# Performance work log

Measured on AMD Instinct MI355X. Metric: run time of the kernel, lower is better.

## Reference

```python
import jax, jax.numpy as jnp
import numpy as np

N = 100000   # nodes (single node type 'A')
C = 256      # hidden_channels
OUT = 128    # out_channels
E_RAND = 300000  # random edges; total E = N + E_RAND = 400000
LN_EPS = 1e-5


def _linear_params(key, in_c, out_c):
    kw, kb = jax.random.split(key)
    bound = 1.0 / np.sqrt(in_c)
    W = jax.random.uniform(kw, (out_c, in_c), minval=-bound, maxval=bound, dtype=jnp.float32)
    b = jax.random.uniform(kb, (out_c,), minval=-bound, maxval=bound, dtype=jnp.float32)
    return W, b


def _edges(key):
    # guarantee every node appears in both rows -> unique()/remap in the torch
    # code is the identity, so the subgraph equals the full graph
    k0, k1 = jax.random.split(key)
    base = jnp.arange(N, dtype=jnp.int64)
    row0 = jnp.concatenate([base, jax.random.randint(k0, (E_RAND,), 0, N, dtype=jnp.int64)])
    row1 = jnp.concatenate([base, jax.random.randint(k1, (E_RAND,), 0, N, dtype=jnp.int64)])
    return jnp.stack([row0, row1])


def setup_inputs() -> dict:
    key = jax.random.key(0)
    ks = jax.random.split(key, 12)
    x = jax.random.normal(ks[0], (N, C), dtype=jnp.float32)
    edge_index_r0 = _edges(ks[1])
    edge_index_r1 = _edges(ks[2])
    wl0, bl0 = _linear_params(ks[3], C, C)
    w00, b00 = _linear_params(ks[4], C, C)
    w10, b10 = _linear_params(ks[5], C, C)
    wl1, bl1 = _linear_params(ks[6], C, C)
    w01, b01 = _linear_params(ks[7], C, C)
    w11, b11 = _linear_params(ks[8], C, C)
    Wout, bout = _linear_params(ks[9], C, OUT)
    return dict(
        x=x, edge_index_r0=edge_index_r0, edge_index_r1=edge_index_r1,
        wl0=wl0, bl0=bl0, w00=w00, b00=b00, w10=w10, b10=b10,
        gate0=jnp.float32(0.5), lns0=jnp.ones((C,), jnp.float32), lnb0=jnp.zeros((C,), jnp.float32),
        wl1=wl1, bl1=bl1, w01=w01, b01=b01, w11=w11, b11=b11,
        gate1=jnp.float32(0.5), lns1=jnp.ones((C,), jnp.float32), lnb1=jnp.zeros((C,), jnp.float32),
        Wout=Wout, bout=bout,
    )


def _metapath_layer(x0, h, ei, wl, bl, w0, b0, w1, b1, gate, lns, lnb):
    n = h.shape[0]
    src, dst = ei[0], ei[1]
    # PyG flow='target_to_source', aggr='add': message x_j = h[edge_index[1]],
    # scatter-added at edge_index[0]
    agg = jax.ops.segment_sum(h[dst], src, num_segments=n)
    # original code normalizes by bincount of edge_index[1] (kept faithfully)
    deg = jax.ops.segment_sum(jnp.ones_like(dst, dtype=h.dtype), dst, num_segments=n)
    agg = agg / jnp.clip(deg, 1.0)[:, None]
    g = jax.nn.sigmoid(gate)
    out = (agg @ wl.T + bl) + (1.0 - g) * (h @ w0.T + b0) + g * (x0 @ w1.T + b1)
    out = jax.nn.relu(out)
    mu = out.mean(-1, keepdims=True)
    var = out.var(-1, keepdims=True)
    out = (out - mu) / jnp.sqrt(var + LN_EPS) * lns + lnb
    return out  # dropout is identity in eval mode


def reference(x, edge_index_r0, edge_index_r1,
              wl0, bl0, w00, b00, w10, b10, gate0, lns0, lnb0,
              wl1, bl1, w01, b01, w11, b11, gate1, lns1, lnb1,
              Wout, bout):
    x0 = jax.lax.stop_gradient(x)  # x0_dict is detached in the torch code
    h = x
    # metapath is processed in reverse: conv index 1 first, then conv index 0
    h = _metapath_layer(x0, h, edge_index_r1, wl1, bl1, w01, b01, w11, b11, gate1, lns1, lnb1)
    h = _metapath_layer(x0, h, edge_index_r0, wl0, bl0, w00, b00, w10, b10, gate0, lns0, lnb0)
    return h @ Wout.T + bout
```

## Files before the change

### kernel.cpp

```cpp
#include <hip/hip_runtime.h>

typedef unsigned short u16;
typedef unsigned int   u32;

typedef __attribute__((ext_vector_type(8))) __bf16 bf16x8;
typedef __attribute__((ext_vector_type(8))) unsigned short u16x8;
typedef __attribute__((ext_vector_type(4))) float  f32x4;

#define C      256
#define KCAT   768
#define OUTC   128
#define LN_EPS 1e-5f

__device__ __forceinline__ float bf2f(u16 u) {
    u32 i = ((u32)u) << 16; float f; __builtin_memcpy(&f, &i, 4); return f;
}
__device__ __forceinline__ u16 f2bf(float f) {
    u32 i; __builtin_memcpy(&i, &f, 4);
    u32 r = (i + 0x7FFFu + ((i >> 16) & 1u)) >> 16;
    return (u16)r;
}
__device__ __forceinline__ void load_lds16(const void* g, void* l) {
    __builtin_amdgcn_global_load_lds((const __attribute__((address_space(1))) u32*)g,
                                     (__attribute__((address_space(3))) u32*)l, 16, 0, 0);
}

__global__ void prep_weights(const float* wlA, const float* w0A, const float* w1A,
                             const float* blA, const float* b0A, const float* b1A,
                             const float* gateA,
                             const float* wlB, const float* w0B, const float* w1B,
                             const float* blB, const float* b0B, const float* b1B,
                             const float* gateB,
                             const float* Wout,
                             u16* __restrict__ Wcat, float* __restrict__ bcat,
                             u16* __restrict__ Woutb)
{
    int idx = blockIdx.x * 256 + threadIdx.x;
    if (idx < 2 * C * KCAT) {
        int L   = idx / (C * KCAT);
        int rem = idx - L * (C * KCAT);
        int n   = rem / KCAT;
        int k   = rem - n * KCAT;
        const float* wl = L ? wlB : wlA;
        const float* w0 = L ? w0B : w0A;
        const float* w1 = L ? w1B : w1A;
        float g = 1.f / (1.f + expf(-((L ? gateB : gateA)[0])));
        float v;
        if (k < 256)      v = wl[n * 256 + k];
        else if (k < 512) v = (1.f - g) * w0[n * 256 + (k - 256)];
        else              v = g * w1[n * 256 + (k - 512)];
        Wcat[idx] = f2bf(v);
        if (idx < 2 * C) {
            int LL = idx / C, nn = idx & 255;
            float gg = 1.f / (1.f + expf(-((LL ? gateB : gateA)[0])));
            bcat[idx] = (LL ? blB : blA)[nn]
                      + (1.f - gg) * (LL ? b0B : b0A)[nn]
                      + gg * (LL ? b1B : b1A)[nn];
        }
    } else {
        int j = idx - 2 * C * KCAT;
        if (j < OUTC * C) Woutb[j] = f2bf(Wout[j]);
    }
}

__global__ void count_edges(const int* __restrict__ ei, int* __restrict__ counts,
                            int* __restrict__ degcnt, int E, int Nn)
{
    int idx = blockIdx.x * 256 + threadIdx.x;
    if (idx >= E) return;
    int s = ei[idx], d = ei[E + idx];
    if ((unsigned)s >= (unsigned)Nn || (unsigned)d >= (unsigned)Nn) return;
    atomicAdd(counts + s, 1);
    atomicAdd(degcnt + d, 1);
}

__global__ void block_sums(const int* __restrict__ counts, int* __restrict__ partials, int n)
{
    int i = blockIdx.x * 256 + threadIdx.x;
    int v = (i < n) ? counts[i] : 0;
    #pragma unroll
    for (int off = 32; off; off >>= 1) v += __shfl_down(v, off, 64);
    __shared__ int ws[4];
    if ((threadIdx.x & 63) == 0) ws[threadIdx.x >> 6] = v;
    __syncthreads();
    if (threadIdx.x == 0) partials[blockIdx.x] = ws[0] + ws[1] + ws[2] + ws[3];
}

__global__ void scan_partials(int* __restrict__ partials, int nblk)
{
    __shared__ int buf[1024];
    int tid = threadIdx.x;
    int v = (tid < nblk) ? partials[tid] : 0;
    buf[tid] = v; __syncthreads();
    for (int off = 1; off < 1024; off <<= 1) {
        int t = (tid >= off) ? buf[tid - off] : 0;
        __syncthreads();
        buf[tid] += t;
        __syncthreads();
    }
    if (tid < nblk) partials[tid] = buf[tid] - v;
}

__global__ void make_offsets(int* __restrict__ counts_cursor, const int* __restrict__ partials,
                             int* __restrict__ offsets, int n)
{
    __shared__ int buf[256];
    int i = blockIdx.x * 256 + threadIdx.x;
    int cnt = (i < n) ? counts_cursor[i] : 0;
    buf[threadIdx.x] = cnt; __syncthreads();
    for (int off = 1; off < 256; off <<= 1) {
        int t = (threadIdx.x >= off) ? buf[threadIdx.x - off] : 0;
        __syncthreads();
        buf[threadIdx.x] += t;
        __syncthreads();
    }
    int off = partials[blockIdx.x] + buf[threadIdx.x] - cnt;
    if (i < n) {
        offsets[i] = off;
        counts_cursor[i] = off;
        if (i == n - 1) offsets[n] = off + cnt;
    }
}

__global__ void fill_edges(const int* __restrict__ ei, int* __restrict__ cursor,
                           int* __restrict__ edgedst, int E, int Nn)
{
    int idx = blockIdx.x * 256 + threadIdx.x;
    if (idx >= E) return;
    int s = ei[idx], d = ei[E + idx];
    if ((unsigned)s >= (unsigned)Nn || (unsigned)d >= (unsigned)Nn) return;
    int p = atomicAdd(cursor + s, 1);
    edgedst[p] = d;
}

template <bool H_BF16>
__global__ __launch_bounds__(256) void gather_kernel(
    const int* __restrict__ offsets, const int* __restrict__ edgedst,
    const int* __restrict__ degcnt, const void* __restrict__ h_,
    u16* __restrict__ aggb, int Nn)
{
    int node = blockIdx.x * 4 + (threadIdx.x >> 6);
    if (node >= Nn) return;
    int lane = threadIdx.x & 63;
    int beg = offsets[node], end = offsets[node + 1];
    float4 acc = {0.f, 0.f, 0.f, 0.f};
    if (H_BF16) {
        const u16* h = (const u16*)h_;
        for (int e = beg; e < end; ++e) {
            int dst = edgedst[e];
            ushort4 v = *(const ushort4*)(h + (size_t)dst * C + lane * 4);
            acc.x += bf2f(v.x); acc.y += bf2f(v.y);
            acc.z += bf2f(v.z); acc.w += bf2f(v.w);
        }
    } else {
        const float* h = (const float*)h_;
        for (int e = beg; e < end; ++e) {
            int dst = edgedst[e];
            float4 v = *(const float4*)(h + (size_t)dst * C + lane * 4);
            acc.x += v.x; acc.y += v.y; acc.z += v.z; acc.w += v.w;
        }
    }
    float inv = 1.0f / fmaxf((float)degcnt[node], 1.0f);
    ushort4 o;
    o.x = f2bf(acc.x * inv); o.y = f2bf(acc.y * inv);
    o.z = f2bf(acc.z * inv); o.w = f2bf(acc.w * inv);
    *(ushort4*)(aggb + (size_t)node * C + lane * 4) = o;
}

template <bool H_BF16>
__global__ __launch_bounds__(256) void layer_gemm(
    const u16* __restrict__ Aagg,
    const void* __restrict__ Ah_, const float* __restrict__ Ax,
    const u16* __restrict__ W,
    const float* __restrict__ bcat,
    const float* __restrict__ lns, const float* __restrict__ lnb,
    u16* __restrict__ Hout, int Nnodes)
{
    __shared__ u16 Alds[64 * 32];
    __shared__ u16 Blds[256 * 32];
    __shared__ float lnpart[64][2][2];

    const int tid = threadIdx.x;
    const int wave = tid >> 6, lane = tid & 63;
    const int wave_m = wave & 1, wave_n = wave >> 1;
    const int q = lane >> 4, l15 = lane & 15;
    const int m0 = blockIdx.x * 64;

    int a_row  = wave * 16 + (lane >> 2);
    int a_node = m0 + a_row; if (a_node >= Nnodes) a_node = Nnodes - 1;
    const int kk8 = (lane & 3) * 8;
    const size_t a_off = (size_t)a_node * C + kk8;
    u16* AldsW = Alds + wave * 512;

    const u16* bg[4]; u16* bl[4];
    #pragma unroll
    for (int i = 0; i < 4; ++i) {
        int cb = wave * 4 + i;
        int n_row = cb * 16 + (lane >> 2);
        bg[i] = W + n_row * KCAT + kk8;
        bl[i] = Blds + cb * 512;
    }

    f32x4 acc[2][8] = {};

    for (int kt = 0; kt < 24; ++kt) {
        int k0 = kt * 32;
        const float* fsrc = nullptr;
        if (kt < 8) {
            load_lds16(Aagg + a_off + k0, AldsW);
        } else if (kt < 16) {
            if (H_BF16) load_lds16((const u16*)Ah_ + a_off + (k0 & 255), AldsW);
            else        fsrc = (const float*)Ah_ + a_off + (k0 & 255);
        } else {
            fsrc = Ax + a_off + (k0 & 255);
        }
        if (fsrc) {
            float4 v0 = *(const float4*)(fsrc);
            float4 v1 = *(const float4*)(fsrc + 4);
            u16x8 o;
            o[0] = f2bf(v0.x); o[1] = f2bf(v0.y); o[2] = f2bf(v0.z); o[3] = f2bf(v0.w);
            o[4] = f2bf(v1.x); o[5] = f2bf(v1.y); o[6] = f2bf(v1.z); o[7] = f2bf(v1.w);
            *(u16x8*)(AldsW + lane * 8) = o;
        }
        #pragma unroll
        for (int i = 0; i < 4; ++i) load_lds16(bg[i] + k0, bl[i]);
        __syncthreads();

        bf16x8 af[2], bfr[8];
        #pragma unroll
        for (int t = 0; t < 2; ++t)
            af[t] = *(const bf16x8*)&Alds[(wave_m * 32 + t * 16 + l15) * 32 + q * 8];
        #pragma unroll
        for (int f = 0; f < 8; ++f)
            bfr[f] = *(const bf16x8*)&Blds[(wave_n * 128 + f * 16 + l15) * 32 + q * 8];
        #pragma unroll
        for (int t = 0; t < 2; ++t)
            #pragma unroll
            for (int f = 0; f < 8; ++f)
                acc[t][f] = __builtin_amdgcn_mfma_f32_16x16x32_bf16(af[t], bfr[f], acc[t][f], 0, 0, 0);
        __syncthreads();
    }

    float bias[8], lsc[8], lbi[8];
    #pragma unroll
    for (int f = 0; f < 8; ++f) {
        int n = wave_n * 128 + f * 16 + l15;
        bias[f] = bcat[n]; lsc[f] = lns[n]; lbi[f] = lnb[n];
    }
    float s1[2][4], s2[2][4];
    #pragma unroll
    for (int t = 0; t < 2; ++t)
        #pragma unroll
        for (int r = 0; r < 4; ++r) {
            float p = 0.f, pp = 0.f;
            #pragma unroll
            for (int f = 0; f < 8; ++f) {
                float v = acc[t][f][r] + bias[f];
                v = fmaxf(v, 0.f);
                acc[t][f][r] = v;
                p += v; pp += v * v;
            }
            #pragma unroll
            for (int off = 1; off < 16; off <<= 1) {
                p  += __shfl_xor(p,  off, 16);
                pp += __shfl_xor(pp, off, 16);
            }
            s1[t][r] = p; s2[t][r] = pp;
        }
    if (l15 == 0) {
        #pragma unroll
        for (int t = 0; t < 2; ++t)
            #pragma unroll
            for (int r = 0; r < 4; ++r) {
                int row = wave_m * 32 + t * 16 + q * 4 + r;
                lnpart[row][wave_n][0] = s1[t][r];
                lnpart[row][wave_n][1] = s2[t][r];
            }
    }
    __syncthreads();
    #pragma unroll
    for (int t = 0; t < 2; ++t)
        #pragma unroll
        for (int r = 0; r < 4; ++r) {
            int row = wave_m * 32 + t * 16 + q * 4 + r;
            int node = m0 + row;
            if (node < Nnodes) {
                float S1 = lnpart[row][0][0] + lnpart[row][1][0];
                float S2 = lnpart[row][0][1] + lnpart[row][1][1];
                float mean = S1 * (1.f / 256.f);
                float var  = S2 * (1.f / 256.f) - mean * mean;
                var = fmaxf(var, 0.f);
                float rstd = rsqrtf(var + LN_EPS);
                u16* op = Hout + (size_t)node * C;
                #pragma unroll
                for (int f = 0; f < 8; ++f) {
                    int n = wave_n * 128 + f * 16 + l15;
                    op[n] = f2bf((acc[t][f][r] - mean) * rstd * lsc[f] + lbi[f]);
                }
            }
        }
}

__global__ __launch_bounds__(256) void final_gemm(
    const u16* __restrict__ A, const u16* __restrict__ W,
    const float* __restrict__ bout, float* __restrict__ out, int Nnodes)
{
    __shared__ u16 Alds[64 * 32];
    __shared__ u16 Blds[128 * 32];

    const int tid = threadIdx.x;
    const int wave = tid >> 6, lane = tid & 63;
    const int wave_m = wave & 1, wave_n = wave >> 1;
    const int q = lane >> 4, l15 = lane & 15;
    const int m0 = blockIdx.x * 64;

    int a_row  = wave * 16 + (lane >> 2);
    int a_node = m0 + a_row; if (a_node >= Nnodes) a_node = Nnodes - 1;
    const int kk8 = (lane & 3) * 8;
    const size_t a_off = (size_t)a_node * C + kk8;
    u16* AldsW = Alds + wave * 512;

    const u16* bg[2]; u16* bl[2];
    #pragma unroll
    for (int i = 0; i < 2; ++i) {
        int cb = wave * 2 + i;
        int n_row = cb * 16 + (lane >> 2);
        bg[i] = W + n_row * 256 + kk8;
        bl[i] = Blds + cb * 512;
    }

    f32x4 acc[2][4] = {};

    for (int kt = 0; kt < 8; ++kt) {
        int k0 = kt * 32;
        load_lds16(A + a_off + k0, AldsW);
        #pragma unroll
        for (int i = 0; i < 2; ++i) load_lds16(bg[i] + k0, bl[i]);
        __syncthreads();

        bf16x8 af[2], bfr[4];
        #pragma unroll
        for (int t = 0; t < 2; ++t)
            af[t] = *(const bf16x8*)&Alds[(wave_m * 32 + t * 16 + l15) * 32 + q * 8];
        #pragma unroll
        for (int f = 0; f < 4; ++f)
            bfr[f] = *(const bf16x8*)&Blds[(wave_n * 64 + f * 16 + l15) * 32 + q * 8];
        #pragma unroll
        for (int t = 0; t < 2; ++t)
            #pragma unroll
            for (int f = 0; f < 4; ++f)
                acc[t][f] = __builtin_amdgcn_mfma_f32_16x16x32_bf16(af[t], bfr[f], acc[t][f], 0, 0, 0);
        __syncthreads();
    }

    float bias[4];
    #pragma unroll
    for (int f = 0; f < 4; ++f) bias[f] = bout[wave_n * 64 + f * 16 + l15];
    #pragma unroll
    for (int t = 0; t < 2; ++t)
        #pragma unroll
        for (int r = 0; r < 4; ++r) {
            int row = wave_m * 32 + t * 16 + q * 4 + r;
            int node = m0 + row;
            if (node < Nnodes) {
                float* op = out + (size_t)node * OUTC;
                #pragma unroll
                for (int f = 0; f < 4; ++f) {
                    int n = wave_n * 64 + f * 16 + l15;
                    op[n] = acc[t][f][r] + bias[f];
                }
            }
        }
}

extern "C" void kernel_launch(void* const* d_in, const int* in_sizes, int n_in,
                              void* d_out, int out_size, void* d_ws, size_t ws_size,
                              hipStream_t stream)
{
    const float* x    = (const float*)d_in[0];
    const int*   ei0  = (const int*)d_in[1];
    const int*   ei1  = (const int*)d_in[2];
    const float* wl0  = (const float*)d_in[3];
    const float* bl0  = (const float*)d_in[4];
    const float* w00  = (const float*)d_in[5];
    const float* b00  = (const float*)d_in[6];
    const float* w10  = (const float*)d_in[7];
    const float* b10  = (const float*)d_in[8];
    const float* gate0= (const float*)d_in[9];
    const float* lns0 = (const float*)d_in[10];
    const float* lnb0 = (const float*)d_in[11];
    const float* wl1  = (const float*)d_in[12];
    const float* bl1  = (const float*)d_in[13];
    const float* w01  = (const float*)d_in[14];
    const float* b01  = (const float*)d_in[15];
    const float* w11  = (const float*)d_in[16];
    const float* b11  = (const float*)d_in[17];
    const float* gate1= (const float*)d_in[18];
    const float* lns1 = (const float*)d_in[19];
    const float* lnb1 = (const float*)d_in[20];
    const float* Wout = (const float*)d_in[21];
    const float* bout = (const float*)d_in[22];

    const int N = in_sizes[0] / C;
    const int E = in_sizes[1] / 2;

    char* w = (char*)d_ws;
    u16*   Wcat  = (u16*)w;   w += (size_t)2 * C * KCAT * 2;
    u16*   Woutb = (u16*)w;   w += (size_t)OUTC * C * 2;
    float* bcat  = (float*)w; w += 4096;
    int*   cnt1  = (int*)w;   w += (size_t)N * 4;
    int*   deg1  = (int*)w;   w += (size_t)N * 4;
    int*   cnt0  = (int*)w;   w += (size_t)N * 4;
    int*   deg0  = (int*)w;   w += (size_t)N * 4;
    int*   off1  = (int*)w;   w += (((size_t)(N + 1) * 4) + 255) & ~255ull;
    int*   off0  = (int*)w;   w += (((size_t)(N + 1) * 4) + 255) & ~255ull;
    int*   parts = (int*)w;   w += 4096;
    int*   ed1   = (int*)w;   w += (size_t)E * 4;
    int*   ed0   = (int*)w;   w += (size_t)E * 4;
    u16*   aggb  = (u16*)w;   w += (size_t)N * C * 2;
    u16*   h1    = (u16*)w;   w += (size_t)N * C * 2;

    const int eb_grid = (E + 255) / 256;
    const int nblk    = (N + 255) / 256;
    const int gt_grid = (N + 3) / 4;
    const int gm_grid = (N + 63) / 64;
    u16* h2 = (u16*)d_out;

    hipMemsetAsync(cnt1, 0, (size_t)4 * N * 4, stream);
    prep_weights<<<(2 * C * KCAT + OUTC * C) / 256, 256, 0, stream>>>(
        wl1, w01, w11, bl1, b01, b11, gate1,
        wl0, w00, w10, bl0, b00, b10, gate0,
        Wout, Wcat, bcat, Woutb);

    count_edges<<<eb_grid, 256, 0, stream>>>(ei1, cnt1, deg1, E, N);
    count_edges<<<eb_grid, 256, 0, stream>>>(ei0, cnt0, deg0, E, N);
    block_sums<<<nblk, 256, 0, stream>>>(cnt1, parts, N);
    scan_partials<<<1, 1024, 0, stream>>>(parts, nblk);
    make_offsets<<<nblk, 256, 0, stream>>>(cnt1, parts, off1, N);
    fill_edges<<<eb_grid, 256, 0, stream>>>(ei1, cnt1, ed1, E, N);
    block_sums<<<nblk, 256, 0, stream>>>(cnt0, parts, N);
    scan_partials<<<1, 1024, 0, stream>>>(parts, nblk);
    make_offsets<<<nblk, 256, 0, stream>>>(cnt0, parts, off0, N);
    fill_edges<<<eb_grid, 256, 0, stream>>>(ei0, cnt0, ed0, E, N);

    gather_kernel<false><<<gt_grid, 256, 0, stream>>>(off1, ed1, deg1, x, aggb, N);
    layer_gemm<false><<<gm_grid, 256, 0, stream>>>(aggb, x, x, Wcat, bcat,
                                                   lns1, lnb1, h1, N);

    gather_kernel<true><<<gt_grid, 256, 0, stream>>>(off0, ed0, deg0, h1, aggb, N);
    layer_gemm<true><<<gm_grid, 256, 0, stream>>>(aggb, h1, x, Wcat + C * KCAT,
                                                  bcat + C, lns0, lnb0, h2, N);

    final_gemm<<<gm_grid, 256, 0, stream>>>(h2, Woutb, bout, (float*)d_out, N);
}
```

Before: 658.1 us.

## Pre-cast x to bf16, fold first-layer weights, enlarge GEMM tile with LDS swizzle

Adds a kernel that converts x to bf16 once, so the gather and both layer GEMMs read bf16 through direct global-to-LDS loads instead of converting fp32 per tile. Because h equals x0 in the first layer, the two self weights are summed into one block and that GEMM shrinks from K=768 to K=512. The layer GEMM moves to 128-row tiles with 512 threads, a 4x4 MFMA accumulator per wave and an XOR-swizzled LDS layout meant to avoid bank conflicts. The cost is an extra pass and buffer for bf16 x, and more register pressure from the larger tile.

```diff
diff --git a/kernel.cpp b/kernel.cpp
--- a/kernel.cpp
+++ b/kernel.cpp
@@ -8,7 +8,6 @@
 typedef __attribute__((ext_vector_type(4))) float  f32x4;
 
 #define C      256
-#define KCAT   768
 #define OUTC   128
 #define LN_EPS 1e-5f
 
@@ -24,42 +23,56 @@
     __builtin_amdgcn_global_load_lds((const __attribute__((address_space(1))) u32*)g,
                                      (__attribute__((address_space(3))) u32*)l, 16, 0, 0);
 }
-
-__global__ void prep_weights(const float* wlA, const float* w0A, const float* w1A,
-                             const float* blA, const float* b0A, const float* b1A,
-                             const float* gateA,
-                             const float* wlB, const float* w0B, const float* w1B,
-                             const float* blB, const float* b0B, const float* b1B,
-                             const float* gateB,
+__device__ __forceinline__ int swz(int row) { return (row + (row >> 2)) & 3; }
+
+__global__ void xcast_kernel(const float* __restrict__ x, u16* __restrict__ xb, size_t n8)
+{
+    size_t i = ((size_t)blockIdx.x * 256 + threadIdx.x);
+    if (i >= n8) return;
+    const float* p = x + i * 8;
+    float4 v0 = *(const float4*)p;
+    float4 v1 = *(const float4*)(p + 4);
+    u16x8 o;
+    o[0] = f2bf(v0.x); o[1] = f2bf(v0.y); o[2] = f2bf(v0.z); o[3] = f2bf(v0.w);
+    o[4] = f2bf(v1.x); o[5] = f2bf(v1.y); o[6] = f2bf(v1.z); o[7] = f2bf(v1.w);
+    *(u16x8*)(xb + i * 8) = o;
+}
+
+__global__ void prep_weights(const float* wl0, const float* w00, const float* w10,
+                             const float* bl0, const float* b00, const float* b10,
+                             const float* gate0,
+                             const float* wl1, const float* w01, const float* w11,
+                             const float* bl1, const float* b01, const float* b11,
+                             const float* gate1,
                              const float* Wout,
-                             u16* __restrict__ Wcat, float* __restrict__ bcat,
-                             u16* __restrict__ Woutb)
+                             u16* __restrict__ WcatA, u16* __restrict__ WcatB,
+                             u16* __restrict__ Woutb, float* __restrict__ bcat)
 {
     int idx = blockIdx.x * 256 + threadIdx.x;
-    if (idx < 2 * C * KCAT) {
-        int L   = idx / (C * KCAT);
-        int rem = idx - L * (C * KCAT);
-        int n   = rem / KCAT;
-        int k   = rem - n * KCAT;
-        const float* wl = L ? wlB : wlA;
-        const float* w0 = L ? w0B : w0A;
-        const float* w1 = L ? w1B : w1A;
-        float g = 1.f / (1.f + expf(-((L ? gateB : gateA)[0])));
+    float gA = 1.f / (1.f + expf(-gate1[0]));
+    float gB = 1.f / (1.f + expf(-gate0[0]));
+    if (idx < 256 * 512) {
+        int n = idx >> 9, k = idx & 511;
         float v;
-        if (k < 256)      v = wl[n * 256 + k];
-        else if (k < 512) v = (1.f - g) * w0[n * 256 + (k - 256)];
-        else              v = g * w1[n * 256 + (k - 512)];
-        Wcat[idx] = f2bf(v);
-        if (idx < 2 * C) {
-            int LL = idx / C, nn = idx & 255;
-            float gg = 1.f / (1.f + expf(-((LL ? gateB : gateA)[0])));
-            bcat[idx] = (LL ? blB : blA)[nn]
-                      + (1.f - gg) * (LL ? b0B : b0A)[nn]
-                      + gg * (LL ? b1B : b1A)[nn];
-        }
+        if (k < 256) v = wl1[n * 256 + k];
+        else         v = (1.f - gA) * w01[n * 256 + (k - 256)] + gA * w11[n * 256 + (k - 256)];
+        WcatA[idx] = f2bf(v);
+    } else if (idx < 256 * 512 + 256 * 768) {
+        int j = idx - 256 * 512;
+        int n = j / 768, k = j - n * 768;
+        float v;
+        if (k < 256)      v = wl0[n * 256 + k];
+        else if (k < 512) v = (1.f - gB) * w00[n * 256 + (k - 256)];
+        else              v = gB * w10[n * 256 + (k - 512)];
+        WcatB[j] = f2bf(v);
     } else {
-        int j = idx - 2 * C * KCAT;
+        int j = idx - (256 * 512 + 256 * 768);
         if (j < OUTC * C) Woutb[j] = f2bf(Wout[j]);
+    }
+    if (idx < 512) {
+        int nn = idx & 255;
+        if (idx < 256) bcat[idx] = bl1[nn] + (1.f - gA) * b01[nn] + gA * b11[nn];
+        else           bcat[idx] = bl0[nn] + (1.f - gB) * b00[nn] + gB * b10[nn];
     }
 }
 
@@ -133,10 +146,9 @@
     edgedst[p] = d;
 }
 
-template <bool H_BF16>
 __global__ __launch_bounds__(256) void gather_kernel(
     const int* __restrict__ offsets, const int* __restrict__ edgedst,
-    const int* __restrict__ degcnt, const void* __restrict__ h_,
+    const int* __restrict__ degcnt, const u16* __restrict__ h,
     u16* __restrict__ aggb, int Nn)
 {
     int node = blockIdx.x * 4 + (threadIdx.x >> 6);
@@ -144,21 +156,11 @@
     int lane = threadIdx.x & 63;
     int beg = offsets[node], end = offsets[node + 1];
     float4 acc = {0.f, 0.f, 0.f, 0.f};
-    if (H_BF16) {
-        const u16* h = (const u16*)h_;
-        for (int e = beg; e < end; ++e) {
-            int dst = edgedst[e];
-            ushort4 v = *(const ushort4*)(h + (size_t)dst * C + lane * 4);
-            acc.x += bf2f(v.x); acc.y += bf2f(v.y);
-            acc.z += bf2f(v.z); acc.w += bf2f(v.w);
-        }
-    } else {
-        const float* h = (const float*)h_;
-        for (int e = beg; e < end; ++e) {
-            int dst = edgedst[e];
-            float4 v = *(const float4*)(h + (size_t)dst * C + lane * 4);
-            acc.x += v.x; acc.y += v.y; acc.z += v.z; acc.w += v.w;
-        }
+    for (int e = beg; e < end; ++e) {
+        int dst = edgedst[e];
+        ushort4 v = *(const ushort4*)(h + (size_t)dst * C + lane * 4);
+        acc.x += bf2f(v.x); acc.y += bf2f(v.y);
+        acc.z += bf2f(v.z); acc.w += bf2f(v.w);
     }
     float inv = 1.0f / fmaxf((float)degcnt[node], 1.0f);
     ushort4 o;
@@ -167,94 +169,88 @@
     *(ushort4*)(aggb + (size_t)node * C + lane * 4) = o;
 }
 
-template <bool H_BF16>
-__global__ __launch_bounds__(256) void layer_gemm(
-    const u16* __restrict__ Aagg,
-    const void* __restrict__ Ah_, const float* __restrict__ Ax,
+template <int NSEG>
+__global__ __launch_bounds__(512, 4) void layer_gemm(
+    const u16* __restrict__ s0, const u16* __restrict__ s1, const u16* __restrict__ s2,
     const u16* __restrict__ W,
     const float* __restrict__ bcat,
     const float* __restrict__ lns, const float* __restrict__ lnb,
     u16* __restrict__ Hout, int Nnodes)
 {
-    __shared__ u16 Alds[64 * 32];
+    constexpr int WK = NSEG * 256;
+    constexpr int KT = NSEG * 8;
+
+    __shared__ u16 Alds[128 * 32];
     __shared__ u16 Blds[256 * 32];
-    __shared__ float lnpart[64][2][2];
-
-    const int tid = threadIdx.x;
+    __shared__ float lnpart[128][4][2];
+
+    const int tid  = threadIdx.x;
     const int wave = tid >> 6, lane = tid & 63;
     const int wave_m = wave & 1, wave_n = wave >> 1;
     const int q = lane >> 4, l15 = lane & 15;
-    const int m0 = blockIdx.x * 64;
-
-    int a_row  = wave * 16 + (lane >> 2);
-    int a_node = m0 + a_row; if (a_node >= Nnodes) a_node = Nnodes - 1;
-    const int kk8 = (lane & 3) * 8;
-    const size_t a_off = (size_t)a_node * C + kk8;
-    u16* AldsW = Alds + wave * 512;
-
-    const u16* bg[4]; u16* bl[4];
-    #pragma unroll
-    for (int i = 0; i < 4; ++i) {
-        int cb = wave * 4 + i;
-        int n_row = cb * 16 + (lane >> 2);
-        bg[i] = W + n_row * KCAT + kk8;
-        bl[i] = Blds + cb * 512;
-    }
-
-    f32x4 acc[2][8] = {};
-
-    for (int kt = 0; kt < 24; ++kt) {
-        int k0 = kt * 32;
-        const float* fsrc = nullptr;
-        if (kt < 8) {
-            load_lds16(Aagg + a_off + k0, AldsW);
-        } else if (kt < 16) {
-            if (H_BF16) load_lds16((const u16*)Ah_ + a_off + (k0 & 255), AldsW);
-            else        fsrc = (const float*)Ah_ + a_off + (k0 & 255);
-        } else {
-            fsrc = Ax + a_off + (k0 & 255);
-        }
-        if (fsrc) {
-            float4 v0 = *(const float4*)(fsrc);
-            float4 v1 = *(const float4*)(fsrc + 4);
-            u16x8 o;
-            o[0] = f2bf(v0.x); o[1] = f2bf(v0.y); o[2] = f2bf(v0.z); o[3] = f2bf(v0.w);
-            o[4] = f2bf(v1.x); o[5] = f2bf(v1.y); o[6] = f2bf(v1.z); o[7] = f2bf(v1.w);
-            *(u16x8*)(AldsW + lane * 8) = o;
-        }
-        #pragma unroll
-        for (int i = 0; i < 4; ++i) load_lds16(bg[i] + k0, bl[i]);
-        __syncthreads();
-
-        bf16x8 af[2], bfr[8];
-        #pragma unroll
-        for (int t = 0; t < 2; ++t)
-            af[t] = *(const bf16x8*)&Alds[(wave_m * 32 + t * 16 + l15) * 32 + q * 8];
-        #pragma unroll
-        for (int f = 0; f < 8; ++f)
-            bfr[f] = *(const bf16x8*)&Blds[(wave_n * 128 + f * 16 + l15) * 32 + q * 8];
-        #pragma unroll
-        for (int t = 0; t < 2; ++t)
+    const int m0 = blockIdx.x * 128;
+
+    const int srow = (wave << 4) + (lane >> 2);
+    int anode = m0 + srow; if (anode >= Nnodes) anode = Nnodes - 1;
+    const int asc = (lane & 3) ^ swz(srow);
+    const size_t a_goff = (size_t)anode * C + asc * 8;
+    u16* a_ldst = Alds + (wave << 9);
+
+    const u16* bgp[2]; u16* bldst[2];
+    #pragma unroll
+    for (int i = 0; i < 2; ++i) {
+        int cb = wave + i * 8;
+        int brow = (cb << 4) + (lane >> 2);
+        int bsc = (lane & 3) ^ swz(brow);
+        bgp[i]   = W + brow * WK + bsc * 8;
+        bldst[i] = Blds + (cb << 9);
+    }
+
+    int aoff[4], boff[4];
+    #pragma unroll
+    for (int t = 0; t < 4; ++t) {
+        int ar = wave_m * 64 + t * 16 + l15;
+        aoff[t] = ar * 32 + ((q ^ swz(ar)) << 3);
+        int br = wave_n * 64 + t * 16 + l15;
+        boff[t] = br * 32 + ((q ^ swz(br)) << 3);
+    }
+
+    f32x4 acc[4][4] = {};
+
+    for (int kt = 0; kt < KT; ++kt) {
+        const u16* Asrc = (kt < 8) ? s0 : ((NSEG == 2 || kt < 16) ? s1 : s2);
+        load_lds16(Asrc + a_goff + ((kt & 7) << 5), a_ldst);
+        int k0 = kt << 5;
+        load_lds16(bgp[0] + k0, bldst[0]);
+        load_lds16(bgp[1] + k0, bldst[1]);
+        __syncthreads();
+
+        bf16x8 af[4], bfr[4];
+        #pragma unroll
+        for (int t = 0; t < 4; ++t) af[t]  = *(const bf16x8*)&Alds[aoff[t]];
+        #pragma unroll
+        for (int f = 0; f < 4; ++f) bfr[f] = *(const bf16x8*)&Blds[boff[f]];
+        #pragma unroll
+        for (int t = 0; t < 4; ++t)
             #pragma unroll
-            for (int f = 0; f < 8; ++f)
+            for (int f = 0; f < 4; ++f)
                 acc[t][f] = __builtin_amdgcn_mfma_f32_16x16x32_bf16(af[t], bfr[f], acc[t][f], 0, 0, 0);
         __syncthreads();
     }
 
-    float bias[8], lsc[8], lbi[8];
-    #pragma unroll
-    for (int f = 0; f < 8; ++f) {
-        int n = wave_n * 128 + f * 16 + l15;
+    float bias[4], lsc[4], lbi[4];
+    #pragma unroll
+    for (int f = 0; f < 4; ++f) {
+        int n = wave_n * 64 + f * 16 + l15;
         bias[f] = bcat[n]; lsc[f] = lns[n]; lbi[f] = lnb[n];
     }
-    float s1[2][4], s2[2][4];
-    #pragma unroll
-    for (int t = 0; t < 2; ++t)
+    #pragma unroll
+    for (int t = 0; t < 4; ++t)
         #pragma unroll
         for (int r = 0; r < 4; ++r) {
             float p = 0.f, pp = 0.f;
             #pragma unroll
-            for (int f = 0; f < 8; ++f) {
+            for (int f = 0; f < 4; ++f) {
                 float v = acc[t][f][r] + bias[f];
                 v = fmaxf(v, 0.f);
                 acc[t][f][r] = v;
@@ -265,36 +261,31 @@
                 p  += __shfl_xor(p,  off, 16);
                 pp += __shfl_xor(pp, off, 16);
             }
-            s1[t][r] = p; s2[t][r] = pp;
+            if (l15 == 0) {
+                int row = wave_m * 64 + t * 16 + q * 4 + r;
+                lnpart[row][wave_n][0] = p;
+                lnpart[row][wave_n][1] = pp;
+            }
         }
-    if (l15 == 0) {
-        #pragma unroll
-        for (int t = 0; t < 2; ++t)
-            #pragma unroll
-            for (int r = 0; r < 4; ++r) {
-                int row = wave_m * 32 + t * 16 + q * 4 + r;
-                lnpart[row][wave_n][0] = s1[t][r];
-                lnpart[row][wave_n][1] = s2[t][r];
-            }
-    }
     __syncthreads();
     #pragma unroll
-    for (int t = 0; t < 2; ++t)
+    for (int t = 0; t < 4; ++t)
         #pragma unroll
         for (int r = 0; r < 4; ++r) {
-            int row = wave_m * 32 + t * 16 + q * 4 + r;
+            int row = wave_m * 64 + t * 16 + q * 4 + r;
             int node = m0 + row;
             if (node < Nnodes) {
-                float S1 = lnpart[row][0][0] + lnpart[row][1][0];
-                float S2 = lnpart[row][0][1] + lnpart[row][1][1];
+                float S1 = lnpart[row][0][0] + lnpart[row][1][0]
+                         + lnpart[row][2][0] + lnpart[row][3][0];
+                float S2 = lnpart[row][0][1] + lnpart[row][1][1]
+                         + lnpart[row][2][1] + lnpart[row][3][1];
                 float mean = S1 * (1.f / 256.f);
-                float var  = S2 * (1.f / 256.f) - mean * mean;
-                var = fmaxf(var, 0.f);
+                float var  = fmaxf(S2 * (1.f / 256.f) - mean * mean, 0.f);
                 float rstd = rsqrtf(var + LN_EPS);
                 u16* op = Hout + (size_t)node * C;
                 #pragma unroll
-                for (int f = 0; f < 8; ++f) {
-                    int n = wave_n * 128 + f * 16 + l15;
+                for (int f = 0; f < 4; ++f) {
+                    int n = wave_n * 64 + f * 16 + l15;
                     op[n] = f2bf((acc[t][f][r] - mean) * rstd * lsc[f] + lbi[f]);
                 }
             }
@@ -405,7 +396,8 @@
     const int E = in_sizes[1] / 2;
 
     char* w = (char*)d_ws;
-    u16*   Wcat  = (u16*)w;   w += (size_t)2 * C * KCAT * 2;
+    u16*   WcatA = (u16*)w;   w += (size_t)256 * 512 * 2;
+    u16*   WcatB = (u16*)w;   w += (size_t)256 * 768 * 2;
     u16*   Woutb = (u16*)w;   w += (size_t)OUTC * C * 2;
     float* bcat  = (float*)w; w += 4096;
     int*   cnt1  = (int*)w;   w += (size_t)N * 4;
@@ -417,20 +409,24 @@
     int*   parts = (int*)w;   w += 4096;
     int*   ed1   = (int*)w;   w += (size_t)E * 4;
     int*   ed0   = (int*)w;   w += (size_t)E * 4;
+    u16*   xb    = (u16*)w;   w += (size_t)N * C * 2;
     u16*   aggb  = (u16*)w;   w += (size_t)N * C * 2;
     u16*   h1    = (u16*)w;   w += (size_t)N * C * 2;
 
     const int eb_grid = (E + 255) / 256;
     const int nblk    = (N + 255) / 256;
     const int gt_grid = (N + 3) / 4;
-    const int gm_grid = (N + 63) / 64;
+    const int gm_grid = (N + 127) / 128;
+    const int fg_grid = (N + 63) / 64;
     u16* h2 = (u16*)d_out;
 
     hipMemsetAsync(cnt1, 0, (size_t)4 * N * 4, stream);
-    prep_weights<<<(2 * C * KCAT + OUTC * C) / 256, 256, 0, stream>>>(
+    prep_weights<<<(256 * 512 + 256 * 768 + OUTC * C) / 256, 256, 0, stream>>>(
+        wl0, w00, w10, bl0, b00, b10, gate0,
         wl1, w01, w11, bl1, b01, b11, gate1,
-        wl0, w00, w10, bl0, b00, b10, gate0,
-        Wout, Wcat, bcat, Woutb);
+        Wout, WcatA, WcatB, Woutb, bcat);
+    xcast_kernel<<<(int)(((size_t)N * C / 8 + 255) / 256), 256, 0, stream>>>(
+        x, xb, (size_t)N * C / 8);
 
     count_edges<<<eb_grid, 256, 0, stream>>>(ei1, cnt1, deg1, E, N);
     count_edges<<<eb_grid, 256, 0, stream>>>(ei0, cnt0, deg0, E, N);
@@ -443,13 +439,13 @@
     make_offsets<<<nblk, 256, 0, stream>>>(cnt0, parts, off0, N);
     fill_edges<<<eb_grid, 256, 0, stream>>>(ei0, cnt0, ed0, E, N);
 
-    gather_kernel<false><<<gt_grid, 256, 0, stream>>>(off1, ed1, deg1, x, aggb, N);
-    layer_gemm<false><<<gm_grid, 256, 0, stream>>>(aggb, x, x, Wcat, bcat,
-                                                   lns1, lnb1, h1, N);
-
-    gather_kernel<true><<<gt_grid, 256, 0, stream>>>(off0, ed0, deg0, h1, aggb, N);
-    layer_gemm<true><<<gm_grid, 256, 0, stream>>>(aggb, h1, x, Wcat + C * KCAT,
-                                                  bcat + C, lns0, lnb0, h2, N);
-
-    final_gemm<<<gm_grid, 256, 0, stream>>>(h2, Woutb, bout, (float*)d_out, N);
-}
+    gather_kernel<<<gt_grid, 256, 0, stream>>>(off1, ed1, deg1, xb, aggb, N);
+    layer_gemm<2><<<gm_grid, 512, 0, stream>>>(aggb, xb, nullptr, WcatA, bcat,
+                                               lns1, lnb1, h1, N);
+
+    gather_kernel<<<gt_grid, 256, 0, stream>>>(off0, ed0, deg0, h1, aggb, N);
+    layer_gemm<3><<<gm_grid, 512, 0, stream>>>(aggb, h1, xb, WcatB, bcat + C,
+                                               lns0, lnb0, h2, N);
+
+    final_gemm<<<fg_grid, 256, 0, stream>>>(h2, Woutb, bout, (float*)d_out, N);
+}
```

Result: faster. 592.3 us (-10.0%).
